# Performance work log

Measured on AMD Instinct MI355X. Metric: run time of the kernel, lower is better.

Reference implementation:

```python
import jax, jax.numpy as jnp
import numpy as np

B, N, D, H, DK, DV, HID, L = 64, 512, 128, 8, 16, 16, 512, 3


def _attention(xq, xk, xv, Wq, Wk, Wv, Wo, mask=None):
    b, nq, _ = xq.shape
    nk = xk.shape[1]
    dk = Wq.shape[1] // H
    dv = Wv.shape[1] // H
    qs = (xq @ Wq).reshape(b, nq, H, dk).transpose(0, 2, 1, 3)   # [b,H,nq,dk]
    ks = (xk @ Wk).reshape(b, nk, H, dk).transpose(0, 2, 1, 3)   # [b,H,nk,dk]
    vs = (xv @ Wv).reshape(b, nk, H, dv).transpose(0, 2, 1, 3)   # [b,H,nk,dv]
    u = jnp.einsum('bhqd,bhkd->bhqk', qs, ks) / (float(dk) ** 0.5)
    if mask is not None:
        u = jnp.where(mask[:, None, None, :], -jnp.inf, u)
    a = jax.nn.softmax(u, axis=-1)
    att = jnp.einsum('bhqk,bhkd->bhqd', a, vs).transpose(0, 2, 1, 3).reshape(b, nq, H * dv)
    return att @ Wo


def _ln(x, g, b):
    mu = x.mean(-1, keepdims=True)
    var = ((x - mu) ** 2).mean(-1, keepdims=True)
    return (x - mu) / jnp.sqrt(var + 1e-6) * g + b


def setup_inputs() -> dict:
    key = jax.random.key(0)
    ks = jax.random.split(key, 32)
    s = 0.02
    def rn(k, shape):
        return jax.random.normal(k, shape, jnp.float32) * s
    return {
        'problems': jax.random.normal(ks[0], (B, N, 2), jnp.float32),
        'embed_W': rn(ks[1], (2, D)),
        'embed_b': jnp.zeros((D,), jnp.float32),
        'enc_Wq': rn(ks[2], (L, D, H * DK)),
        'enc_Wk': rn(ks[3], (L, D, H * DK)),
        'enc_Wv': rn(ks[4], (L, D, H * DV)),
        'enc_Wo': rn(ks[5], (L, H * DV, D)),
        'enc_ln1_g': jnp.ones((L, D), jnp.float32),
        'enc_ln1_b': jnp.zeros((L, D), jnp.float32),
        'enc_ff_W1': rn(ks[6], (L, D, HID)),
        'enc_ff_b1': jnp.zeros((L, HID), jnp.float32),
        'enc_ff_W2': rn(ks[7], (L, HID, D)),
        'enc_ff_b2': jnp.zeros((L, D), jnp.float32),
        'enc_ln2_g': jnp.ones((L, D), jnp.float32),
        'enc_ln2_b': jnp.zeros((L, D), jnp.float32),
        'graph_W': rn(ks[8], (D, D)),
        'node_W': rn(ks[9], (D, D)),
        'dec_Wq': rn(ks[10], (3 * D, H * DK)),
        'dec_Wk': rn(ks[11], (D, H * DK)),
        'dec_Wv': rn(ks[12], (D, H * DV)),
        'dec_Wo': rn(ks[13], (H * DV, D)),
        'W_v_f': jax.random.uniform(ks[14], (1, 1, D), jnp.float32),
        'W_v_l': jax.random.uniform(ks[15], (1, 1, D), jnp.float32),
    }


def reference(problems, embed_W, embed_b, enc_Wq, enc_Wk, enc_Wv, enc_Wo,
              enc_ln1_g, enc_ln1_b, enc_ff_W1, enc_ff_b1, enc_ff_W2, enc_ff_b2,
              enc_ln2_g, enc_ln2_b, graph_W, node_W,
              dec_Wq, dec_Wk, dec_Wv, dec_Wo, W_v_f, W_v_l):
    # --- encoder ---
    x = problems @ embed_W + embed_b
    for i in range(L):
        x = _ln(x + _attention(x, x, x, enc_Wq[i], enc_Wk[i], enc_Wv[i], enc_Wo[i]),
                enc_ln1_g[i], enc_ln1_b[i])
        h = jax.nn.relu(x @ enc_ff_W1[i] + enc_ff_b1[i]) @ enc_ff_W2[i] + enc_ff_b2[i]
        x = _ln(x + h, enc_ln2_g[i], enc_ln2_b[i])
    node_context = x                                             # [B,N,D]
    graph_context = node_context.mean(axis=1, keepdims=True) @ graph_W  # [B,1,D]
    k_node = node_context @ node_W                               # loop-invariant, hoisted
    first0 = jnp.broadcast_to(W_v_f, (B, 1, D))
    last0 = jnp.broadcast_to(W_v_l, (B, 1, D))
    mask0 = jnp.zeros((B, N), bool)
    step_keys = jax.random.split(jax.random.key(42), N)
    batch_idx = jnp.arange(B)

    def step(carry, inp):
        mask, last, first = carry
        i, k = inp
        cq = jnp.concatenate([graph_context, last, first], axis=-1)   # [B,1,3D]
        q = _attention(cq, node_context, node_context, dec_Wq, dec_Wk, dec_Wv, dec_Wo, mask)  # [B,1,D]
        logits = jnp.einsum('bqd,bnd->bqn', q, k_node)[:, 0, :] / (float(D) ** 0.5)
        logits = jnp.where(mask, -jnp.inf, jnp.tanh(logits) * 10.0)
        actions = jax.random.categorical(k, logits)                   # [B]
        probs = jax.nn.softmax(logits, axis=-1)
        p = jnp.take_along_axis(probs, actions[:, None], axis=1)[:, 0]
        mask = mask.at[batch_idx, actions].set(True)
        # faithful to original: gather index is [1,B,D], so it reads batch 0's node_context
        new_last = node_context[0][actions][:, None, :]               # [B,1,D]
        first = jnp.where(i == 0, new_last, first)
        return (mask, new_last, first), (p, actions)

    _, (probs_seq, actions_seq) = jax.lax.scan(
        step, (mask0, last0, first0), (jnp.arange(N), step_keys))
    return probs_seq, actions_seq
```

## Files before the change

### kernel.cpp

```cpp
#include <hip/hip_runtime.h>


#define NEGINF (-__builtin_huge_valf())
#define TINYF 1.17549435e-38f

__device__ __forceinline__ unsigned rotl32(unsigned v, int r) {
  return (v << r) | (v >> (32 - r));
}

__device__ __forceinline__ void threefry2x32(unsigned k0, unsigned k1,
                                             unsigned& x0, unsigned& x1) {
  unsigned k2 = k0 ^ k1 ^ 0x1BD11BDAu;
  x0 += k0; x1 += k1;
#define TF_R(r) { x0 += x1; x1 = rotl32(x1, (r)); x1 ^= x0; }
  TF_R(13) TF_R(15) TF_R(26) TF_R(6)
  x0 += k1; x1 += k2 + 1u;
  TF_R(17) TF_R(29) TF_R(16) TF_R(24)
  x0 += k2; x1 += k0 + 2u;
  TF_R(13) TF_R(15) TF_R(26) TF_R(6)
  x0 += k0; x1 += k1 + 3u;
  TF_R(17) TF_R(29) TF_R(16) TF_R(24)
  x0 += k1; x1 += k2 + 4u;
  TF_R(13) TF_R(15) TF_R(26) TF_R(6)
  x0 += k2; x1 += k0 + 5u;
#undef TF_R
}

__device__ __forceinline__ float4 f4fma(float s, float4 v, float4 a) {
  a.x += s * v.x; a.y += s * v.y; a.z += s * v.z; a.w += s * v.w; return a;
}

__global__ __launch_bounds__(256) void k_embed(const float* __restrict__ P,
                                               const float* __restrict__ eW,
                                               const float* __restrict__ eb,
                                               float* __restrict__ X) {
  int idx = blockIdx.x * 256 + threadIdx.x;
  int row = idx >> 7, d = idx & 127;
  X[idx] = P[row * 2] * eW[d] + P[row * 2 + 1] * eW[128 + d] + eb[d];
}

__global__ __launch_bounds__(256) void k_gemm128(const float* __restrict__ A,
                                                 const float* __restrict__ W,
                                                 const float* __restrict__ R,
                                                 float* __restrict__ C, int M) {
  __shared__ float As[16][129];
  __shared__ float Ws[128][17];
  const int tx = threadIdx.x & 15, ty = threadIdx.x >> 4;
  const int row0 = blockIdx.x * 16, col0 = blockIdx.y * 16;
  for (int idx = threadIdx.x; idx < 2048; idx += 256) {
    int r = idx >> 7, k = idx & 127;
    As[r][k] = (row0 + r < M) ? A[(size_t)(row0 + r) * 128 + k] : 0.0f;
    int kk = idx >> 4, c = idx & 15;
    Ws[kk][c] = W[(size_t)kk * 128 + col0 + c];
  }
  __syncthreads();
  float acc = 0.0f;
#pragma unroll 8
  for (int k = 0; k < 128; ++k) acc += As[ty][k] * Ws[k][tx];
  const int row = row0 + ty, col = col0 + tx;
  if (row < M) {
    if (R) acc += R[(size_t)row * 128 + col];
    C[(size_t)row * 128 + col] = acc;
  }
}

#define GEP_BIAS 1
#define GEP_RELU 2
#define GEP_ADDR 4
#define GEP_ACC  8
#define GEP_TST  16
#define GEP_WT   32

__global__ __launch_bounds__(256, 2) void k_gemm64(
    const float* __restrict__ A, int lda,
    const float* __restrict__ W, int ldw,
    const float* __restrict__ bias,
    const float* __restrict__ R,
    float* __restrict__ C, int ldc,
    int K, int flags) {
  __shared__ float AsT[128 * 68];
  __shared__ float Bs[128 * 68];
  const int t = threadIdx.x;
  const int tx = t & 15, ty = t >> 4;
  const int row0 = blockIdx.x * 64, col0 = blockIdx.y * 64;
  float4 acc[4];
  acc[0] = acc[1] = acc[2] = acc[3] = make_float4(0.f, 0.f, 0.f, 0.f);

  for (int K0 = 0; K0 < K; K0 += 128) {
    if (K0) __syncthreads();
#pragma unroll
    for (int j = 0; j < 8; ++j) {
      int idx = t + j * 256;
      int r = idx & 63, kq = idx >> 6;
      float4 v = *(const float4*)&A[(size_t)(row0 + r) * lda + K0 + kq * 4];
      AsT[(kq * 4 + 0) * 68 + r] = v.x;
      AsT[(kq * 4 + 1) * 68 + r] = v.y;
      AsT[(kq * 4 + 2) * 68 + r] = v.z;
      AsT[(kq * 4 + 3) * 68 + r] = v.w;
    }
    if (flags & GEP_WT) {
#pragma unroll
      for (int j = 0; j < 8; ++j) {
        int idx = t + j * 256;
        int cc = idx & 63, kq = idx >> 6;
        float4 v = *(const float4*)&W[(size_t)(col0 + cc) * ldw + K0 + kq * 4];
        Bs[(kq * 4 + 0) * 68 + cc] = v.x;
        Bs[(kq * 4 + 1) * 68 + cc] = v.y;
        Bs[(kq * 4 + 2) * 68 + cc] = v.z;
        Bs[(kq * 4 + 3) * 68 + cc] = v.w;
      }
    } else {
#pragma unroll
      for (int j = 0; j < 8; ++j) {
        int idx = t + j * 256;
        int c4 = idx & 15, k = idx >> 4;
        *(float4*)&Bs[k * 68 + c4 * 4] =
            *(const float4*)&W[(size_t)(K0 + k) * ldw + col0 + c4 * 4];
      }
    }
    __syncthreads();
#pragma unroll 8
    for (int k = 0; k < 128; ++k) {
      float4 av = *(const float4*)&AsT[k * 68 + ty * 4];
      float4 bv = *(const float4*)&Bs[k * 68 + tx * 4];
      acc[0] = f4fma(av.x, bv, acc[0]);
      acc[1] = f4fma(av.y, bv, acc[1]);
      acc[2] = f4fma(av.z, bv, acc[2]);
      acc[3] = f4fma(av.w, bv, acc[3]);
    }
  }

  if (flags & GEP_TST) {
    __syncthreads();
    float* CtT = AsT;
#pragma unroll
    for (int i2 = 0; i2 < 4; ++i2) {
      CtT[(tx * 4 + 0) * 68 + ty * 4 + i2] = ((const float*)&acc[i2])[0];
      CtT[(tx * 4 + 1) * 68 + ty * 4 + i2] = ((const float*)&acc[i2])[1];
      CtT[(tx * 4 + 2) * 68 + ty * 4 + i2] = ((const float*)&acc[i2])[2];
      CtT[(tx * 4 + 3) * 68 + ty * 4 + i2] = ((const float*)&acc[i2])[3];
    }
    __syncthreads();
    for (int j = 0; j < 16; ++j) {
      int idx = t + j * 256;
      int n = idx & 63, c = idx >> 6;
      int grow = row0 + n;
      C[(size_t)(grow >> 9) * 65536 + (size_t)(col0 + c) * 512 + (grow & 511)] =
          CtT[c * 68 + n];
    }
  } else {
#pragma unroll
    for (int i2 = 0; i2 < 4; ++i2) {
      const int row = row0 + ty * 4 + i2, col = col0 + tx * 4;
      float4 v = acc[i2];
      if (flags & GEP_BIAS) {
        float4 b4 = *(const float4*)&bias[col];
        v.x += b4.x; v.y += b4.y; v.z += b4.z; v.w += b4.w;
      }
      if (flags & GEP_RELU) {
        v.x = fmaxf(v.x, 0.f); v.y = fmaxf(v.y, 0.f);
        v.z = fmaxf(v.z, 0.f); v.w = fmaxf(v.w, 0.f);
      }
      if (flags & GEP_ADDR) {
        float4 r4 = *(const float4*)&R[(size_t)row * ldc + col];
        v.x += r4.x; v.y += r4.y; v.z += r4.z; v.w += r4.w;
      }
      if (flags & GEP_ACC) {
        float4 c4 = *(const float4*)&C[(size_t)row * ldc + col];
        v.x += c4.x; v.y += c4.y; v.z += c4.z; v.w += c4.w;
      }
      *(float4*)&C[(size_t)row * ldc + col] = v;
    }
  }
}

__global__ __launch_bounds__(256) void k_repack4(const float* __restrict__ in,
                                                 float* __restrict__ out) {
  int idx = blockIdx.x * 256 + threadIdx.x;
  int n = idx & 511, q = (idx >> 9) & 31, b = idx >> 14;
  const float* ip = in + (size_t)b * 65536 + (size_t)(q * 4) * 512 + n;
  float4 v = make_float4(ip[0], ip[512], ip[1024], ip[1536]);
  *reinterpret_cast<float4*>(out + (size_t)b * 65536 + (size_t)q * 2048 + n * 4) = v;
}

__global__ __launch_bounds__(512, 2) void k_attn_enc(const float* __restrict__ Q,
                                                     const float* __restrict__ K,
                                                     const float* __restrict__ V,
                                                     float* __restrict__ O) {
  const int b = blockIdx.x >> 3, h = blockIdx.x & 7;
  const int t = threadIdx.x, l = t & 63, w = t >> 6;
  __shared__ float4 Vs4[512][5];
  __shared__ float S[32][516];
  __shared__ float Qs[32][16];
  __shared__ float invr[32];
  const size_t base = (size_t)b * 512 * 128 + (size_t)h * 16;
  float4 k0, k1, k2, k3;
  {
    const float4* kr = reinterpret_cast<const float4*>(K + base + (size_t)t * 128);
    k0 = kr[0]; k1 = kr[1]; k2 = kr[2]; k3 = kr[3];
  }
  for (int idx = t; idx < 2048; idx += 512) {
    int n = idx >> 2, c = idx & 3;
    Vs4[n][c] = reinterpret_cast<const float4*>(V + base + (size_t)n * 128)[c];
  }
  __syncthreads();
  const float* vsf = reinterpret_cast<const float*>(Vs4);
  for (int qt = 0; qt < 16; ++qt) {
    { int qr = t >> 4, d = t & 15;
      Qs[qr][d] = Q[base + (size_t)(qt * 32 + qr) * 128 + d]; }
    __syncthreads();
#pragma unroll 4
    for (int qi = 0; qi < 32; ++qi) {
      const float* qv = Qs[qi];
      float s = qv[0] * k0.x + qv[1] * k0.y + qv[2] * k0.z + qv[3] * k0.w
              + qv[4] * k1.x + qv[5] * k1.y + qv[6] * k1.z + qv[7] * k1.w
              + qv[8] * k2.x + qv[9] * k2.y + qv[10] * k2.z + qv[11] * k2.w
              + qv[12] * k3.x + qv[13] * k3.y + qv[14] * k3.z + qv[15] * k3.w;
      S[qi][t] = s * 0.25f;
    }
    __syncthreads();
    for (int r = 0; r < 4; ++r) {
      const int qi = w * 4 + r;
      float m = S[qi][l];
      for (int j = 1; j < 8; ++j) m = fmaxf(m, S[qi][l + 64 * j]);
      for (int o = 32; o; o >>= 1) m = fmaxf(m, __shfl_xor(m, o));
      float sum = 0.0f;
      for (int j = 0; j < 8; ++j) {
        float e = expf(S[qi][l + 64 * j] - m);
        S[qi][l + 64 * j] = e;
        sum += e;
      }
      for (int o = 32; o; o >>= 1) sum += __shfl_xor(sum, o);
      if (l == 0) invr[qi] = 1.0f / sum;
    }
    __syncthreads();
    {
      const int qi = t >> 4, d = t & 15;
      float acc = 0.0f;
      for (int n = 0; n < 512; ++n) acc += S[qi][n] * vsf[n * 20 + d];
      O[base + (size_t)(qt * 32 + qi) * 128 + d] = acc * invr[qi];
    }
  }
}

__global__ __launch_bounds__(256) void k_ln(const float* __restrict__ Y,
                                            const float* __restrict__ g,
                                            const float* __restrict__ bb,
                                            float* __restrict__ O, int M) {
  const int row = blockIdx.x * 4 + (threadIdx.x >> 6);
  const int l = threadIdx.x & 63;
  if (row >= M) return;
  const float* y = Y + (size_t)row * 128;
  float v0 = y[l], v1 = y[l + 64];
  float s = v0 + v1;
  for (int o = 32; o; o >>= 1) s += __shfl_xor(s, o);
  const float mu = s * (1.0f / 128.0f);
  float d0 = v0 - mu, d1 = v1 - mu;
  float q = d0 * d0 + d1 * d1;
  for (int o = 32; o; o >>= 1) q += __shfl_xor(q, o);
  const float sd = sqrtf(q * (1.0f / 128.0f) + 1e-6f);
  O[(size_t)row * 128 + l]      = d0 / sd * g[l] + bb[l];
  O[(size_t)row * 128 + l + 64] = d1 / sd * g[l + 64] + bb[l + 64];
}

__global__ __launch_bounds__(128) void k_mean(const float* __restrict__ X,
                                              float* __restrict__ NM) {
  const int b = blockIdx.x, d = threadIdx.x;
  float s = 0.0f;
  for (int n = 0; n < 512; ++n) s += X[((size_t)b * 512 + n) * 128 + d];
  NM[b * 128 + d] = s * (1.0f / 512.0f);
}

__global__ __launch_bounds__(512, 2) void k_decoder(
    const float* __restrict__ Kt, const float* __restrict__ Vt,
    const float* __restrict__ KnW4,
    const float* __restrict__ QG, const float* __restrict__ QL,
    const float* __restrict__ QF, const float* __restrict__ QL0,
    const float* __restrict__ QF0,
    float* __restrict__ out_probs, float* __restrict__ out_act) {
  const int b = blockIdx.x, t = threadIdx.x;
  const int l = t & 63, w = t >> 6, h = w;

  __shared__ float att_s[128];
  __shared__ float pv[8][64 * 17];
  __shared__ float l_lds[512];
  __shared__ uint2 keys[512];
  __shared__ float redZ[8]; __shared__ int redI[8];
  __shared__ float redM[8]; __shared__ float redD[8];

  {
    unsigned x0 = 0u, x1 = (unsigned)t;
    threefry2x32(0u, 42u, x0, x1);
    keys[t] = make_uint2(x0, x1);
  }
  __syncthreads();

  const float4* KtB = reinterpret_cast<const float4*>(Kt + (size_t)b * 65536);
  const float4* VtB = reinterpret_cast<const float4*>(Vt + (size_t)b * 65536);
  const float4* kn4 = reinterpret_cast<const float4*>(KnW4 + (size_t)b * 65536);

  float4 mk0 = make_float4(0.f, 0.f, 0.f, 0.f);
  float4 mk1 = make_float4(0.f, 0.f, 0.f, 0.f);
  float emask = 0.0f;
  int ap = 0, af = 0;

  float qg = 0.0f, qf_r = 0.0f;
  if (l < 16) qg = QG[b * 128 + h * 16 + l];

  for (int i = 0; i < 512; ++i) {
    float qval = 0.0f;
    if (l < 16) {
      const int c = h * 16 + l;
      const float ql_ = (i == 0) ? QL0[c] : QL[(size_t)ap * 128 + c];
      const float qf_ = (i == 0) ? QF0[c] : qf_r;
      qval = (qg + ql_) + qf_;
    }
    float q[16];
#pragma unroll
    for (int d = 0; d < 16; ++d) q[d] = __shfl(qval, d);
    float4 a0 = make_float4(0.f, 0.f, 0.f, 0.f);
    float4 a1 = make_float4(0.f, 0.f, 0.f, 0.f);
#pragma unroll
    for (int d = 0; d < 16; ++d) {
      a0 = f4fma(q[d], KtB[(h * 16 + d) * 128 + l], a0);
      a1 = f4fma(q[d], KtB[(h * 16 + d) * 128 + 64 + l], a1);
    }
    float4 va[4], vb[4];
#pragma unroll
    for (int u = 0; u < 4; ++u) {
      va[u] = VtB[(h * 16 + u) * 128 + l];
      vb[u] = VtB[(h * 16 + u) * 128 + 64 + l];
    }
    float4 s0, s1;
    s0.x = a0.x * 0.25f + mk0.x;  s0.y = a0.y * 0.25f + mk0.y;
    s0.z = a0.z * 0.25f + mk0.z;  s0.w = a0.w * 0.25f + mk0.w;
    s1.x = a1.x * 0.25f + mk1.x;  s1.y = a1.y * 0.25f + mk1.y;
    s1.z = a1.z * 0.25f + mk1.z;  s1.w = a1.w * 0.25f + mk1.w;
    float mh = fmaxf(fmaxf(fmaxf(s0.x, s0.y), fmaxf(s0.z, s0.w)),
                     fmaxf(fmaxf(s1.x, s1.y), fmaxf(s1.z, s1.w)));
    for (int o = 32; o; o >>= 1) mh = fmaxf(mh, __shfl_xor(mh, o));
    float4 e0, e1;
    e0.x = expf(s0.x - mh); e0.y = expf(s0.y - mh);
    e0.z = expf(s0.z - mh); e0.w = expf(s0.w - mh);
    e1.x = expf(s1.x - mh); e1.y = expf(s1.y - mh);
    e1.z = expf(s1.z - mh); e1.w = expf(s1.w - mh);
    float sden = ((e0.x + e0.y) + (e0.z + e0.w)) + ((e1.x + e1.y) + (e1.z + e1.w));
    for (int o = 32; o; o >>= 1) sden += __shfl_xor(sden, o);
    const float inv = 1.0f / sden;
    float ps[16];
#pragma unroll
    for (int u = 0; u < 4; ++u) {
      ps[u] = e0.x * va[u].x + e0.y * va[u].y + e0.z * va[u].z + e0.w * va[u].w
            + e1.x * vb[u].x + e1.y * vb[u].y + e1.z * vb[u].z + e1.w * vb[u].w;
    }
#pragma unroll
    for (int dg = 1; dg < 4; ++dg) {
#pragma unroll
      for (int u = 0; u < 4; ++u) {
        va[u] = VtB[(h * 16 + dg * 4 + u) * 128 + l];
        vb[u] = VtB[(h * 16 + dg * 4 + u) * 128 + 64 + l];
      }
#pragma unroll
      for (int u = 0; u < 4; ++u) {
        ps[dg * 4 + u] = e0.x * va[u].x + e0.y * va[u].y + e0.z * va[u].z + e0.w * va[u].w
                       + e1.x * vb[u].x + e1.y * vb[u].y + e1.z * vb[u].z + e1.w * vb[u].w;
      }
    }
#pragma unroll
    for (int d = 0; d < 16; ++d) pv[w][l * 17 + d] = ps[d];
    asm volatile("s_waitcnt lgkmcnt(0)" ::: "memory");
    float sum = 0.0f;
#pragma unroll
    for (int j = 0; j < 16; ++j)
      sum += pv[w][((l >> 4) * 16 + j) * 17 + (l & 15)];
    sum += __shfl_xor(sum, 16);
    sum += __shfl_xor(sum, 32);
    if (l < 16) att_s[h * 16 + l] = sum * inv;
    float4 kq[8];
#pragma unroll
    for (int q4 = 0; q4 < 8; ++q4) kq[q4] = kn4[q4 * 512 + t];
    __syncthreads();
    float lg, zv;
    {
      const float4* att4 = reinterpret_cast<const float4*>(att_s);
      float acc = 0.0f, acc2 = 0.0f;
#pragma unroll
      for (int q4 = 0; q4 < 8; ++q4) {
        const float4 av = att4[q4];
        const float4 kv = kq[q4];
        acc  += av.x * kv.x;  acc  += av.y * kv.y;
        acc2 += av.z * kv.z;  acc2 += av.w * kv.w;
      }
#pragma unroll 8
      for (int q4 = 8; q4 < 32; ++q4) {
        const float4 av = att4[q4];
        const float4 kv = kn4[q4 * 512 + t];
        acc  += av.x * kv.x;  acc  += av.y * kv.y;
        acc2 += av.z * kv.z;  acc2 += av.w * kv.w;
      }
      const float lraw = (acc + acc2) / 11.313708498984761f;
      lg = tanhf(lraw) * 10.0f + emask;
      l_lds[t] = lg;
      unsigned x0 = 0u, x1 = (unsigned)(b * 512 + t);
      const uint2 kk = keys[i];
      threefry2x32(kk.x, kk.y, x0, x1);
      const unsigned bits = x0 ^ x1;
      float f = __uint_as_float((bits >> 9) | 0x3f800000u) - 1.0f;
      f = f + TINYF;
      f = fmaxf(TINYF, f);
      zv = lg + (-logf(-logf(f)));
    }
    {
      float z = zv; int zi = t;
      float mm = lg;
      for (int o = 32; o; o >>= 1) {
        float oz = __shfl_xor(z, o); int oi = __shfl_xor(zi, o);
        if (oz > z || (oz == z && oi < zi)) { z = oz; zi = oi; }
        mm = fmaxf(mm, __shfl_xor(mm, o));
      }
      float e = expf(lg - mm);
      for (int o = 32; o; o >>= 1) e += __shfl_xor(e, o);
      if (l == 0) { redZ[w] = z; redI[w] = zi; redM[w] = mm; redD[w] = e; }
    }
    __syncthreads();
    float bz = redZ[0]; int a = redI[0]; float M = redM[0];
#pragma unroll
    for (int ww = 1; ww < 8; ++ww) {
      float oz = redZ[ww]; int oi = redI[ww];
      if (oz > bz || (oz == bz && oi < a)) { bz = oz; a = oi; }
      M = fmaxf(M, redM[ww]);
    }
    if (t == 0) {
      float den = 0.0f;
#pragma unroll
      for (int ww = 0; ww < 8; ++ww) {
        float mw = redM[ww];
        if (mw != NEGINF) den += redD[ww] * expf(mw - M);
      }
      out_probs[i * 64 + b] = expf(l_lds[a] - M) / den;
      out_act[i * 64 + b] = (float)a;
    }
    ap = a;
    if (i == 0) {
      af = a;
      if (l < 16) qf_r = QF[(size_t)a * 128 + h * 16 + l];
    }
    const int n0 = l << 2;
    mk0.x = (a == n0)       ? NEGINF : mk0.x;
    mk0.y = (a == n0 + 1)   ? NEGINF : mk0.y;
    mk0.z = (a == n0 + 2)   ? NEGINF : mk0.z;
    mk0.w = (a == n0 + 3)   ? NEGINF : mk0.w;
    mk1.x = (a == 256 + n0)     ? NEGINF : mk1.x;
    mk1.y = (a == 256 + n0 + 1) ? NEGINF : mk1.y;
    mk1.z = (a == 256 + n0 + 2) ? NEGINF : mk1.z;
    mk1.w = (a == 256 + n0 + 3) ? NEGINF : mk1.w;
    emask = (a == t) ? NEGINF : emask;
  }
}

extern "C" void kernel_launch(void* const* d_in, const int* in_sizes, int n_in,
                              void* d_out, int out_size, void* d_ws, size_t ws_size,
                              hipStream_t stream) {
  const float* problems = (const float*)d_in[0];
  const float* embed_W  = (const float*)d_in[1];
  const float* embed_b  = (const float*)d_in[2];
  const float* enc_Wq   = (const float*)d_in[3];
  const float* enc_Wk   = (const float*)d_in[4];
  const float* enc_Wv   = (const float*)d_in[5];
  const float* enc_Wo   = (const float*)d_in[6];
  const float* ln1g     = (const float*)d_in[7];
  const float* ln1b     = (const float*)d_in[8];
  const float* ffW1     = (const float*)d_in[9];
  const float* ffb1     = (const float*)d_in[10];
  const float* ffW2     = (const float*)d_in[11];
  const float* ffb2     = (const float*)d_in[12];
  const float* ln2g     = (const float*)d_in[13];
  const float* ln2b     = (const float*)d_in[14];
  const float* graph_W  = (const float*)d_in[15];
  const float* node_W   = (const float*)d_in[16];
  const float* dec_Wq   = (const float*)d_in[17];
  const float* dec_Wk   = (const float*)d_in[18];
  const float* dec_Wv   = (const float*)d_in[19];
  const float* dec_Wo   = (const float*)d_in[20];
  const float* W_v_f    = (const float*)d_in[21];
  const float* W_v_l    = (const float*)d_in[22];

  float* ws = (float*)d_ws;
  const size_t SZ = (size_t)64 * 512 * 128;
  float* X  = ws;
  float* Y  = ws + SZ;
  float* Qb = ws + 2 * SZ;
  float* Kb = ws + 3 * SZ;
  float* Vb = ws + 4 * SZ;
  float* NM = ws + 5 * SZ;
  float* GC = NM + 64 * 128;

  float* QG  = Y;
  float* QL  = Y + 8192;
  float* QF  = Y + 8192 + 65536;
  float* QL0 = Y + 8192 + 131072;
  float* QF0 = QL0 + 128;

  float* out       = (float*)d_out;
  float* out_probs = out;
  float* out_act   = out + 512 * 64;

  k_embed<<<16384, 256, 0, stream>>>(problems, embed_W, embed_b, X);

  for (int i = 0; i < 3; ++i) {
    const float* Wqi = enc_Wq + (size_t)i * 16384;
    const float* Wki = enc_Wk + (size_t)i * 16384;
    const float* Wvi = enc_Wv + (size_t)i * 16384;
    const float* Woi = enc_Wo + (size_t)i * 16384;
    k_gemm64<<<dim3(512, 2), 256, 0, stream>>>(X, 128, Wqi, 128, nullptr, nullptr, Qb, 128, 128, 0);
    k_gemm64<<<dim3(512, 2), 256, 0, stream>>>(X, 128, Wki, 128, nullptr, nullptr, Kb, 128, 128, 0);
    k_gemm64<<<dim3(512, 2), 256, 0, stream>>>(X, 128, Wvi, 128, nullptr, nullptr, Vb, 128, 128, 0);
    k_attn_enc<<<512, 512, 0, stream>>>(Qb, Kb, Vb, Y);
    k_gemm64<<<dim3(512, 2), 256, 0, stream>>>(Y, 128, Woi, 128, nullptr, X, Qb, 128, 128, GEP_ADDR);
    k_ln<<<8192, 256, 0, stream>>>(Qb, ln1g + i * 128, ln1b + i * 128, X, 32768);
    float* H = Kb;
    for (int half = 0; half < 2; ++half) {
      k_gemm64<<<dim3(512, 4), 256, 0, stream>>>(
          X, 128, ffW1 + (size_t)i * 65536 + half * 256, 512,
          ffb1 + i * 512 + half * 256, nullptr, H, 256, 128, GEP_BIAS | GEP_RELU);
      k_gemm64<<<dim3(512, 2), 256, 0, stream>>>(
          H, 256, ffW2 + (size_t)i * 65536 + (size_t)half * 32768, 128,
          ffb2 + i * 128, X, Y, 128, 256,
          half == 0 ? (GEP_BIAS | GEP_ADDR) : GEP_ACC);
    }
    k_ln<<<8192, 256, 0, stream>>>(Y, ln2g + i * 128, ln2b + i * 128, X, 32768);
  }

  k_mean<<<64, 128, 0, stream>>>(X, NM);
  k_gemm128<<<dim3(4, 8), 256, 0, stream>>>(NM, graph_W, nullptr, GC, 64);
  k_gemm128<<<dim3(4, 8), 256, 0, stream>>>(GC, dec_Wq, nullptr, QG, 64);
  k_gemm64<<<dim3(8, 2), 256, 0, stream>>>(X, 128, dec_Wq + 16384, 128, nullptr, nullptr, QL, 128, 128, 0);
  k_gemm64<<<dim3(8, 2), 256, 0, stream>>>(X, 128, dec_Wq + 32768, 128, nullptr, nullptr, QF, 128, 128, 0);
  k_gemm128<<<dim3(1, 8), 256, 0, stream>>>(W_v_l, dec_Wq + 16384, nullptr, QL0, 1);
  k_gemm128<<<dim3(1, 8), 256, 0, stream>>>(W_v_f, dec_Wq + 32768, nullptr, QF0, 1);
  k_gemm64<<<dim3(512, 2), 256, 0, stream>>>(X, 128, dec_Wk, 128, nullptr, nullptr, Qb, 128, 128, GEP_TST);
  k_gemm64<<<dim3(512, 2), 256, 0, stream>>>(X, 128, dec_Wv, 128, nullptr, nullptr, Kb, 128, 128, GEP_TST);
  k_gemm64<<<dim3(512, 2), 256, 0, stream>>>(X, 128, node_W, 128, nullptr, nullptr, Vb, 128, 128, 0);
  k_gemm64<<<dim3(512, 2), 256, 0, stream>>>(Vb, 128, dec_Wo, 128, nullptr, nullptr, X, 128, 128,
                                             GEP_WT | GEP_TST);
  k_repack4<<<4096, 256, 0, stream>>>(X, Vb);

  k_decoder<<<64, 512, 0, stream>>>(Qb, Kb, Vb, QG, QL, QF, QL0, QF0,
                                    out_probs, out_act);
}
```

Measured before the change: 10.01 ms.

## Split decoder per batch across four cooperative blocks with global atomic barriers

The sequential decoder moves from one 512-thread block per batch to four 256-thread blocks per batch, launched cooperatively. Each block keeps its two heads' K/V slices in LDS, and the logit and sampling work is spread over the four blocks. Per-step results are exchanged through global buffers, with two atomic spin barriers per step. The aim is to use more CUs and serve K/V from LDS instead of global memory, at the cost of two cross-block global syncs in each of the 512 steps.

```diff
diff --git a/kernel.cpp b/kernel.cpp
--- a/kernel.cpp
+++ b/kernel.cpp
@@ -30,6 +30,14 @@
   a.x += s * v.x; a.y += s * v.y; a.z += s * v.z; a.w += s * v.w; return a;
 }
 
+__device__ __forceinline__ void bar_sync(int* c, int tgt) {
+  __hip_atomic_fetch_add(c, 1, __ATOMIC_RELEASE, __HIP_MEMORY_SCOPE_AGENT);
+  while (__hip_atomic_load(c, __ATOMIC_RELAXED, __HIP_MEMORY_SCOPE_AGENT) < tgt) {
+    __builtin_amdgcn_s_sleep(1);
+  }
+  (void)__hip_atomic_load(c, __ATOMIC_ACQUIRE, __HIP_MEMORY_SCOPE_AGENT);
+}
+
 __global__ __launch_bounds__(256) void k_embed(const float* __restrict__ P,
                                                const float* __restrict__ eW,
                                                const float* __restrict__ eb,
@@ -37,6 +45,10 @@
   int idx = blockIdx.x * 256 + threadIdx.x;
   int row = idx >> 7, d = idx & 127;
   X[idx] = P[row * 2] * eW[d] + P[row * 2 + 1] * eW[128 + d] + eb[d];
+}
+
+__global__ __launch_bounds__(64) void k_zero(int* __restrict__ p) {
+  p[threadIdx.x] = 0;
 }
 
 __global__ __launch_bounds__(256) void k_gemm128(const float* __restrict__ A,
@@ -271,190 +283,208 @@
   NM[b * 128 + d] = s * (1.0f / 512.0f);
 }
 
-__global__ __launch_bounds__(512, 2) void k_decoder(
-    const float* __restrict__ Kt, const float* __restrict__ Vt,
-    const float* __restrict__ KnW4,
-    const float* __restrict__ QG, const float* __restrict__ QL,
-    const float* __restrict__ QF, const float* __restrict__ QL0,
-    const float* __restrict__ QF0,
-    float* __restrict__ out_probs, float* __restrict__ out_act) {
-  const int b = blockIdx.x, t = threadIdx.x;
-  const int l = t & 63, w = t >> 6, h = w;
-
-  __shared__ float att_s[128];
-  __shared__ float pv[8][64 * 17];
-  __shared__ float l_lds[512];
+__global__ __launch_bounds__(256) void k_decoder(
+    const float* Kt, const float* Vt, const float* KnW4,
+    const float* QG, const float* QL, const float* QF,
+    const float* QL0, const float* QF0,
+    float* attBuf, float* lgBuf, float4* recBuf, int* cnt,
+    float* out_probs, float* out_act) {
+  const int blk = blockIdx.x;
+  const int b = blk >> 2, r = blk & 3;
+  const int t = threadIdx.x, l = t & 63, w = t >> 6;
+  const bool scoreW = (w < 2);
+  const int h = 2 * r + w;
+  const int wl = w - 2;
+  const int n = 128 * r + (t - 128);
+
+  __shared__ float4 kLDS[4096];
+  __shared__ float4 vLDS[4096];
+  __shared__ float pv[2][64 * 17];
+  __shared__ float att_s[2][128];
   __shared__ uint2 keys[512];
-  __shared__ float redZ[8]; __shared__ int redI[8];
-  __shared__ float redM[8]; __shared__ float redD[8];
 
   {
-    unsigned x0 = 0u, x1 = (unsigned)t;
-    threefry2x32(0u, 42u, x0, x1);
-    keys[t] = make_uint2(x0, x1);
+    const float4* KtB = reinterpret_cast<const float4*>(Kt + (size_t)b * 65536) + r * 32 * 128;
+    const float4* VtB = reinterpret_cast<const float4*>(Vt + (size_t)b * 65536) + r * 32 * 128;
+    for (int idx = t; idx < 4096; idx += 256) {
+      kLDS[idx] = KtB[idx];
+      vLDS[idx] = VtB[idx];
+    }
+    for (int idx = t; idx < 512; idx += 256) {
+      unsigned x0 = 0u, x1 = (unsigned)idx;
+      threefry2x32(0u, 42u, x0, x1);
+      keys[idx] = make_uint2(x0, x1);
+    }
   }
   __syncthreads();
 
-  const float4* KtB = reinterpret_cast<const float4*>(Kt + (size_t)b * 65536);
-  const float4* VtB = reinterpret_cast<const float4*>(Vt + (size_t)b * 65536);
   const float4* kn4 = reinterpret_cast<const float4*>(KnW4 + (size_t)b * 65536);
+  float* attB = attBuf + b * 128;
+  float* lgB  = lgBuf + b * 512;
+  float4* recB = recBuf + b * 8;
+  int* cb = cnt + b;
 
   float4 mk0 = make_float4(0.f, 0.f, 0.f, 0.f);
   float4 mk1 = make_float4(0.f, 0.f, 0.f, 0.f);
   float emask = 0.0f;
-  int ap = 0, af = 0;
-
+  int ap = 0;
   float qg = 0.0f, qf_r = 0.0f;
-  if (l < 16) qg = QG[b * 128 + h * 16 + l];
+  if (scoreW && l < 16) qg = QG[b * 128 + h * 16 + l];
 
   for (int i = 0; i < 512; ++i) {
-    float qval = 0.0f;
-    if (l < 16) {
-      const int c = h * 16 + l;
-      const float ql_ = (i == 0) ? QL0[c] : QL[(size_t)ap * 128 + c];
-      const float qf_ = (i == 0) ? QF0[c] : qf_r;
-      qval = (qg + ql_) + qf_;
-    }
-    float q[16];
-#pragma unroll
-    for (int d = 0; d < 16; ++d) q[d] = __shfl(qval, d);
-    float4 a0 = make_float4(0.f, 0.f, 0.f, 0.f);
-    float4 a1 = make_float4(0.f, 0.f, 0.f, 0.f);
-#pragma unroll
-    for (int d = 0; d < 16; ++d) {
-      a0 = f4fma(q[d], KtB[(h * 16 + d) * 128 + l], a0);
-      a1 = f4fma(q[d], KtB[(h * 16 + d) * 128 + 64 + l], a1);
-    }
-    float4 va[4], vb[4];
-#pragma unroll
-    for (int u = 0; u < 4; ++u) {
-      va[u] = VtB[(h * 16 + u) * 128 + l];
-      vb[u] = VtB[(h * 16 + u) * 128 + 64 + l];
-    }
-    float4 s0, s1;
-    s0.x = a0.x * 0.25f + mk0.x;  s0.y = a0.y * 0.25f + mk0.y;
-    s0.z = a0.z * 0.25f + mk0.z;  s0.w = a0.w * 0.25f + mk0.w;
-    s1.x = a1.x * 0.25f + mk1.x;  s1.y = a1.y * 0.25f + mk1.y;
-    s1.z = a1.z * 0.25f + mk1.z;  s1.w = a1.w * 0.25f + mk1.w;
-    float mh = fmaxf(fmaxf(fmaxf(s0.x, s0.y), fmaxf(s0.z, s0.w)),
-                     fmaxf(fmaxf(s1.x, s1.y), fmaxf(s1.z, s1.w)));
-    for (int o = 32; o; o >>= 1) mh = fmaxf(mh, __shfl_xor(mh, o));
-    float4 e0, e1;
-    e0.x = expf(s0.x - mh); e0.y = expf(s0.y - mh);
-    e0.z = expf(s0.z - mh); e0.w = expf(s0.w - mh);
-    e1.x = expf(s1.x - mh); e1.y = expf(s1.y - mh);
-    e1.z = expf(s1.z - mh); e1.w = expf(s1.w - mh);
-    float sden = ((e0.x + e0.y) + (e0.z + e0.w)) + ((e1.x + e1.y) + (e1.z + e1.w));
-    for (int o = 32; o; o >>= 1) sden += __shfl_xor(sden, o);
-    const float inv = 1.0f / sden;
-    float ps[16];
-#pragma unroll
-    for (int u = 0; u < 4; ++u) {
-      ps[u] = e0.x * va[u].x + e0.y * va[u].y + e0.z * va[u].z + e0.w * va[u].w
-            + e1.x * vb[u].x + e1.y * vb[u].y + e1.z * vb[u].z + e1.w * vb[u].w;
-    }
-#pragma unroll
-    for (int dg = 1; dg < 4; ++dg) {
-#pragma unroll
-      for (int u = 0; u < 4; ++u) {
-        va[u] = VtB[(h * 16 + dg * 4 + u) * 128 + l];
-        vb[u] = VtB[(h * 16 + dg * 4 + u) * 128 + 64 + l];
-      }
-#pragma unroll
-      for (int u = 0; u < 4; ++u) {
-        ps[dg * 4 + u] = e0.x * va[u].x + e0.y * va[u].y + e0.z * va[u].z + e0.w * va[u].w
-                       + e1.x * vb[u].x + e1.y * vb[u].y + e1.z * vb[u].z + e1.w * vb[u].w;
-      }
-    }
-#pragma unroll
-    for (int d = 0; d < 16; ++d) pv[w][l * 17 + d] = ps[d];
-    asm volatile("s_waitcnt lgkmcnt(0)" ::: "memory");
-    float sum = 0.0f;
-#pragma unroll
-    for (int j = 0; j < 16; ++j)
-      sum += pv[w][((l >> 4) * 16 + j) * 17 + (l & 15)];
-    sum += __shfl_xor(sum, 16);
-    sum += __shfl_xor(sum, 32);
-    if (l < 16) att_s[h * 16 + l] = sum * inv;
     float4 kq[8];
-#pragma unroll
-    for (int q4 = 0; q4 < 8; ++q4) kq[q4] = kn4[q4 * 512 + t];
-    __syncthreads();
-    float lg, zv;
-    {
-      const float4* att4 = reinterpret_cast<const float4*>(att_s);
-      float acc = 0.0f, acc2 = 0.0f;
-#pragma unroll
-      for (int q4 = 0; q4 < 8; ++q4) {
-        const float4 av = att4[q4];
-        const float4 kv = kq[q4];
-        acc  += av.x * kv.x;  acc  += av.y * kv.y;
-        acc2 += av.z * kv.z;  acc2 += av.w * kv.w;
-      }
+    if (scoreW) {
+      float qval = 0.0f;
+      if (l < 16) {
+        const int c = h * 16 + l;
+        const float ql_ = (i == 0) ? QL0[c] : QL[(size_t)ap * 128 + c];
+        const float qf_ = (i == 0) ? QF0[c] : qf_r;
+        qval = (qg + ql_) + qf_;
+      }
+      float q[16];
+#pragma unroll
+      for (int d = 0; d < 16; ++d) q[d] = __shfl(qval, d);
+      float4 a0 = make_float4(0.f, 0.f, 0.f, 0.f);
+      float4 a1 = make_float4(0.f, 0.f, 0.f, 0.f);
+#pragma unroll
+      for (int d = 0; d < 16; ++d) {
+        a0 = f4fma(q[d], kLDS[(w * 16 + d) * 128 + l], a0);
+        a1 = f4fma(q[d], kLDS[(w * 16 + d) * 128 + 64 + l], a1);
+      }
+      float4 s0, s1;
+      s0.x = a0.x * 0.25f + mk0.x;  s0.y = a0.y * 0.25f + mk0.y;
+      s0.z = a0.z * 0.25f + mk0.z;  s0.w = a0.w * 0.25f + mk0.w;
+      s1.x = a1.x * 0.25f + mk1.x;  s1.y = a1.y * 0.25f + mk1.y;
+      s1.z = a1.z * 0.25f + mk1.z;  s1.w = a1.w * 0.25f + mk1.w;
+      float mh = fmaxf(fmaxf(fmaxf(s0.x, s0.y), fmaxf(s0.z, s0.w)),
+                       fmaxf(fmaxf(s1.x, s1.y), fmaxf(s1.z, s1.w)));
+      for (int o = 32; o; o >>= 1) mh = fmaxf(mh, __shfl_xor(mh, o));
+      float4 e0, e1;
+      e0.x = expf(s0.x - mh); e0.y = expf(s0.y - mh);
+      e0.z = expf(s0.z - mh); e0.w = expf(s0.w - mh);
+      e1.x = expf(s1.x - mh); e1.y = expf(s1.y - mh);
+      e1.z = expf(s1.z - mh); e1.w = expf(s1.w - mh);
+      float sden = ((e0.x + e0.y) + (e0.z + e0.w)) + ((e1.x + e1.y) + (e1.z + e1.w));
+      for (int o = 32; o; o >>= 1) sden += __shfl_xor(sden, o);
+      const float inv = 1.0f / sden;
+      float ps[16];
+#pragma unroll
+      for (int dg = 0; dg < 4; ++dg) {
+        float4 va[4], vb[4];
+#pragma unroll
+        for (int u = 0; u < 4; ++u) {
+          va[u] = vLDS[(w * 16 + dg * 4 + u) * 128 + l];
+          vb[u] = vLDS[(w * 16 + dg * 4 + u) * 128 + 64 + l];
+        }
+#pragma unroll
+        for (int u = 0; u < 4; ++u) {
+          ps[dg * 4 + u] = e0.x * va[u].x + e0.y * va[u].y + e0.z * va[u].z + e0.w * va[u].w
+                         + e1.x * vb[u].x + e1.y * vb[u].y + e1.z * vb[u].z + e1.w * vb[u].w;
+        }
+      }
+#pragma unroll
+      for (int d = 0; d < 16; ++d) pv[w][l * 17 + d] = ps[d];
+      asm volatile("s_waitcnt lgkmcnt(0)" ::: "memory");
+      float sum = 0.0f;
+#pragma unroll
+      for (int j = 0; j < 16; ++j)
+        sum += pv[w][((l >> 4) * 16 + j) * 17 + (l & 15)];
+      sum += __shfl_xor(sum, 16);
+      sum += __shfl_xor(sum, 32);
+      if (l < 16) attB[h * 16 + l] = sum * inv;
+    } else {
+#pragma unroll
+      for (int q4 = 0; q4 < 8; ++q4) kq[q4] = kn4[q4 * 512 + n];
+    }
+    __syncthreads();
+    if (t == 0) bar_sync(cb, 4 * (2 * i + 1));
+    __syncthreads();
+    if (!scoreW) {
+      if (l < 32)
+        reinterpret_cast<float4*>(&att_s[wl][0])[l] =
+            reinterpret_cast<const float4*>(attB)[l];
+      const float4* att4 = reinterpret_cast<const float4*>(&att_s[wl][0]);
+      float lg, zv;
+      {
+        float acc = 0.0f, acc2 = 0.0f;
+#pragma unroll
+        for (int q4 = 0; q4 < 8; ++q4) {
+          const float4 av = att4[q4];
+          const float4 kv = kq[q4];
+          acc  += av.x * kv.x;  acc  += av.y * kv.y;
+          acc2 += av.z * kv.z;  acc2 += av.w * kv.w;
+        }
 #pragma unroll 8
-      for (int q4 = 8; q4 < 32; ++q4) {
-        const float4 av = att4[q4];
-        const float4 kv = kn4[q4 * 512 + t];
-        acc  += av.x * kv.x;  acc  += av.y * kv.y;
-        acc2 += av.z * kv.z;  acc2 += av.w * kv.w;
-      }
-      const float lraw = (acc + acc2) / 11.313708498984761f;
-      lg = tanhf(lraw) * 10.0f + emask;
-      l_lds[t] = lg;
-      unsigned x0 = 0u, x1 = (unsigned)(b * 512 + t);
-      const uint2 kk = keys[i];
-      threefry2x32(kk.x, kk.y, x0, x1);
-      const unsigned bits = x0 ^ x1;
-      float f = __uint_as_float((bits >> 9) | 0x3f800000u) - 1.0f;
-      f = f + TINYF;
-      f = fmaxf(TINYF, f);
-      zv = lg + (-logf(-logf(f)));
-    }
-    {
-      float z = zv; int zi = t;
-      float mm = lg;
-      for (int o = 32; o; o >>= 1) {
-        float oz = __shfl_xor(z, o); int oi = __shfl_xor(zi, o);
-        if (oz > z || (oz == z && oi < zi)) { z = oz; zi = oi; }
-        mm = fmaxf(mm, __shfl_xor(mm, o));
-      }
-      float e = expf(lg - mm);
-      for (int o = 32; o; o >>= 1) e += __shfl_xor(e, o);
-      if (l == 0) { redZ[w] = z; redI[w] = zi; redM[w] = mm; redD[w] = e; }
-    }
-    __syncthreads();
-    float bz = redZ[0]; int a = redI[0]; float M = redM[0];
+        for (int q4 = 8; q4 < 32; ++q4) {
+          const float4 av = att4[q4];
+          const float4 kv = kn4[q4 * 512 + n];
+          acc  += av.x * kv.x;  acc  += av.y * kv.y;
+          acc2 += av.z * kv.z;  acc2 += av.w * kv.w;
+        }
+        const float lraw = (acc + acc2) / 11.313708498984761f;
+        lg = tanhf(lraw) * 10.0f + emask;
+        lgB[n] = lg;
+        unsigned x0 = 0u, x1 = (unsigned)(b * 512 + n);
+        const uint2 kk = keys[i];
+        threefry2x32(kk.x, kk.y, x0, x1);
+        const unsigned bits = x0 ^ x1;
+        float f = __uint_as_float((bits >> 9) | 0x3f800000u) - 1.0f;
+        f = f + TINYF;
+        f = fmaxf(TINYF, f);
+        zv = lg + (-logf(-logf(f)));
+      }
+      {
+        float z = zv; int zi = n;
+        float mm = lg;
+        for (int o = 32; o; o >>= 1) {
+          float oz = __shfl_xor(z, o); int oi = __shfl_xor(zi, o);
+          if (oz > z || (oz == z && oi < zi)) { z = oz; zi = oi; }
+          mm = fmaxf(mm, __shfl_xor(mm, o));
+        }
+        float e = expf(lg - mm);
+        for (int o = 32; o; o >>= 1) e += __shfl_xor(e, o);
+        if (l == 0)
+          recB[2 * r + wl] = make_float4(z, __int_as_float(zi), mm, e);
+      }
+    }
+    __syncthreads();
+    if (t == 0) bar_sync(cb, 4 * (2 * i + 2));
+    __syncthreads();
+    float4 rc[8];
+#pragma unroll
+    for (int ww = 0; ww < 8; ++ww) rc[ww] = recB[ww];
+    float bz = rc[0].x; int a = __float_as_int(rc[0].y); float M = rc[0].z;
 #pragma unroll
     for (int ww = 1; ww < 8; ++ww) {
-      float oz = redZ[ww]; int oi = redI[ww];
+      float oz = rc[ww].x; int oi = __float_as_int(rc[ww].y);
       if (oz > bz || (oz == bz && oi < a)) { bz = oz; a = oi; }
-      M = fmaxf(M, redM[ww]);
-    }
-    if (t == 0) {
+      M = fmaxf(M, rc[ww].z);
+    }
+    if (r == 0 && t == 0) {
       float den = 0.0f;
 #pragma unroll
       for (int ww = 0; ww < 8; ++ww) {
-        float mw = redM[ww];
-        if (mw != NEGINF) den += redD[ww] * expf(mw - M);
-      }
-      out_probs[i * 64 + b] = expf(l_lds[a] - M) / den;
+        float mw = rc[ww].z;
+        if (mw != NEGINF) den += rc[ww].w * expf(mw - M);
+      }
+      out_probs[i * 64 + b] = expf(lgB[a] - M) / den;
       out_act[i * 64 + b] = (float)a;
     }
     ap = a;
-    if (i == 0) {
-      af = a;
-      if (l < 16) qf_r = QF[(size_t)a * 128 + h * 16 + l];
-    }
-    const int n0 = l << 2;
-    mk0.x = (a == n0)       ? NEGINF : mk0.x;
-    mk0.y = (a == n0 + 1)   ? NEGINF : mk0.y;
-    mk0.z = (a == n0 + 2)   ? NEGINF : mk0.z;
-    mk0.w = (a == n0 + 3)   ? NEGINF : mk0.w;
-    mk1.x = (a == 256 + n0)     ? NEGINF : mk1.x;
-    mk1.y = (a == 256 + n0 + 1) ? NEGINF : mk1.y;
-    mk1.z = (a == 256 + n0 + 2) ? NEGINF : mk1.z;
-    mk1.w = (a == 256 + n0 + 3) ? NEGINF : mk1.w;
-    emask = (a == t) ? NEGINF : emask;
+    if (i == 0 && scoreW && l < 16) qf_r = QF[(size_t)a * 128 + h * 16 + l];
+    if (scoreW) {
+      const int n0 = l << 2;
+      mk0.x = (a == n0)       ? NEGINF : mk0.x;
+      mk0.y = (a == n0 + 1)   ? NEGINF : mk0.y;
+      mk0.z = (a == n0 + 2)   ? NEGINF : mk0.z;
+      mk0.w = (a == n0 + 3)   ? NEGINF : mk0.w;
+      mk1.x = (a == 256 + n0)     ? NEGINF : mk1.x;
+      mk1.y = (a == 256 + n0 + 1) ? NEGINF : mk1.y;
+      mk1.z = (a == 256 + n0 + 2) ? NEGINF : mk1.z;
+      mk1.w = (a == 256 + n0 + 3) ? NEGINF : mk1.w;
+    } else {
+      emask = (a == n) ? NEGINF : emask;
+    }
   }
 }
 
@@ -500,6 +530,10 @@
   float* QF  = Y + 8192 + 65536;
   float* QL0 = Y + 8192 + 131072;
   float* QF0 = QL0 + 128;
+  float* attBuf = Y + 262144;
+  float* lgBuf  = Y + 262144 + 8192;
+  float* recBuf = Y + 262144 + 8192 + 32768;
+  int*   cnt    = (int*)(Y + 262144 + 8192 + 32768 + 2048);
 
   float* out       = (float*)d_out;
   float* out_probs = out;
@@ -544,7 +578,18 @@
   k_gemm64<<<dim3(512, 2), 256, 0, stream>>>(Vb, 128, dec_Wo, 128, nullptr, nullptr, X, 128, 128,
                                              GEP_WT | GEP_TST);
   k_repack4<<<4096, 256, 0, stream>>>(X, Vb);
-
-  k_decoder<<<64, 512, 0, stream>>>(Qb, Kb, Vb, QG, QL, QF, QL0, QF0,
-                                    out_probs, out_act);
-}
+  k_zero<<<1, 64, 0, stream>>>(cnt);
+
+  {
+    const float *aKt = Qb, *aVt = Kb, *aKn = Vb, *aQG = QG, *aQL = QL,
+                *aQF = QF, *aQL0 = QL0, *aQF0 = QF0;
+    float *aAtt = attBuf, *aLg = lgBuf;
+    float4* aRec = (float4*)recBuf;
+    int* aCnt = cnt;
+    float *aP = out_probs, *aA = out_act;
+    void* args[] = {&aKt, &aVt, &aKn, &aQG, &aQL, &aQF, &aQL0, &aQF0,
+                    &aAtt, &aLg, &aRec, &aCnt, &aP, &aA};
+    hipLaunchCooperativeKernel(reinterpret_cast<const void*>(k_decoder),
+                               dim3(256), dim3(256), args, 0, stream);
+  }
+}
```

Measured after the change: 17.02 ms. +70.1%, slower.

## Transpose V in LDS for vectorized PV and use LDS-only barriers in decoder

Applied to the files above, without the earlier changes.

The encoder attention now stores V transposed in shared memory, so the P·V loop reads S and V rows as float4 with four partial accumulators instead of doing scalar strided reads. In the decoder loop, the node-key loads are issued earlier so they overlap the attention compute. The two per-step __syncthreads are replaced with a barrier that waits only on LDS counters, which avoids draining outstanding global loads. The transposed V writes may cause LDS bank conflicts, and the lighter barrier depends on no global-memory ordering being needed at those points.

```diff
diff --git a/kernel.cpp b/kernel.cpp
--- a/kernel.cpp
+++ b/kernel.cpp
@@ -30,6 +30,12 @@
   a.x += s * v.x; a.y += s * v.y; a.z += s * v.z; a.w += s * v.w; return a;
 }
 
+__device__ __forceinline__ void lds_barrier() {
+  asm volatile("s_waitcnt lgkmcnt(0)" ::: "memory");
+  __builtin_amdgcn_s_barrier();
+  asm volatile("" ::: "memory");
+}
+
 __global__ __launch_bounds__(256) void k_embed(const float* __restrict__ P,
                                                const float* __restrict__ eW,
                                                const float* __restrict__ eb,
@@ -189,8 +195,8 @@
                                                      float* __restrict__ O) {
   const int b = blockIdx.x >> 3, h = blockIdx.x & 7;
   const int t = threadIdx.x, l = t & 63, w = t >> 6;
-  __shared__ float4 Vs4[512][5];
   __shared__ float S[32][516];
+  __shared__ float VsT[16][516];
   __shared__ float Qs[32][16];
   __shared__ float invr[32];
   const size_t base = (size_t)b * 512 * 128 + (size_t)h * 16;
@@ -201,10 +207,13 @@
   }
   for (int idx = t; idx < 2048; idx += 512) {
     int n = idx >> 2, c = idx & 3;
-    Vs4[n][c] = reinterpret_cast<const float4*>(V + base + (size_t)n * 128)[c];
+    float4 v = reinterpret_cast<const float4*>(V + base + (size_t)n * 128)[c];
+    VsT[4 * c + 0][n] = v.x;
+    VsT[4 * c + 1][n] = v.y;
+    VsT[4 * c + 2][n] = v.z;
+    VsT[4 * c + 3][n] = v.w;
   }
   __syncthreads();
-  const float* vsf = reinterpret_cast<const float*>(Vs4);
   for (int qt = 0; qt < 16; ++qt) {
     { int qr = t >> 4, d = t & 15;
       Qs[qr][d] = Q[base + (size_t)(qt * 32 + qr) * 128 + d]; }
@@ -236,8 +245,17 @@
     __syncthreads();
     {
       const int qi = t >> 4, d = t & 15;
-      float acc = 0.0f;
-      for (int n = 0; n < 512; ++n) acc += S[qi][n] * vsf[n * 20 + d];
+      const float4* Srow = reinterpret_cast<const float4*>(&S[qi][0]);
+      const float4* Vrow = reinterpret_cast<const float4*>(&VsT[d][0]);
+      float4 a4 = make_float4(0.f, 0.f, 0.f, 0.f);
+#pragma unroll 8
+      for (int n4 = 0; n4 < 128; ++n4) {
+        const float4 s4 = Srow[n4];
+        const float4 v4 = Vrow[n4];
+        a4.x += s4.x * v4.x; a4.y += s4.y * v4.y;
+        a4.z += s4.z * v4.z; a4.w += s4.w * v4.w;
+      }
+      const float acc = (a4.x + a4.y) + (a4.z + a4.w);
       O[base + (size_t)(qt * 32 + qi) * 128 + d] = acc * invr[qi];
     }
   }
@@ -302,7 +320,7 @@
   float4 mk0 = make_float4(0.f, 0.f, 0.f, 0.f);
   float4 mk1 = make_float4(0.f, 0.f, 0.f, 0.f);
   float emask = 0.0f;
-  int ap = 0, af = 0;
+  int ap = 0;
 
   float qg = 0.0f, qf_r = 0.0f;
   if (l < 16) qg = QG[b * 128 + h * 16 + l];
@@ -325,6 +343,9 @@
       a0 = f4fma(q[d], KtB[(h * 16 + d) * 128 + l], a0);
       a1 = f4fma(q[d], KtB[(h * 16 + d) * 128 + 64 + l], a1);
     }
+    float4 kq[8];
+#pragma unroll
+    for (int q4 = 0; q4 < 8; ++q4) kq[q4] = kn4[q4 * 512 + t];
     float4 va[4], vb[4];
 #pragma unroll
     for (int u = 0; u < 4; ++u) {
@@ -376,10 +397,7 @@
     sum += __shfl_xor(sum, 16);
     sum += __shfl_xor(sum, 32);
     if (l < 16) att_s[h * 16 + l] = sum * inv;
-    float4 kq[8];
-#pragma unroll
-    for (int q4 = 0; q4 < 8; ++q4) kq[q4] = kn4[q4 * 512 + t];
-    __syncthreads();
+    lds_barrier();
     float lg, zv;
     {
       const float4* att4 = reinterpret_cast<const float4*>(att_s);
@@ -422,7 +440,7 @@
       for (int o = 32; o; o >>= 1) e += __shfl_xor(e, o);
       if (l == 0) { redZ[w] = z; redI[w] = zi; redM[w] = mm; redD[w] = e; }
     }
-    __syncthreads();
+    lds_barrier();
     float bz = redZ[0]; int a = redI[0]; float M = redM[0];
 #pragma unroll
     for (int ww = 1; ww < 8; ++ww) {
@@ -441,10 +459,7 @@
       out_act[i * 64 + b] = (float)a;
     }
     ap = a;
-    if (i == 0) {
-      af = a;
-      if (l < 16) qf_r = QF[(size_t)a * 128 + h * 16 + l];
-    }
+    if (i == 0 && l < 16) qf_r = QF[(size_t)a * 128 + h * 16 + l];
     const int n0 = l << 2;
     mk0.x = (a == n0)       ? NEGINF : mk0.x;
     mk0.y = (a == n0 + 1)   ? NEGINF : mk0.y;
```

After: 9.435 ms. 5.7% less time.
